# Kernel optimization log

Measured on AMD Instinct MI355X. Metric: run time of the kernel, lower is better.

The kernel has to match this reference:

```python
import jax, jax.numpy as jnp
import numpy as np

VIDEO_DIM, TEXT_DIM, ATTN_DIM = 1024, 768, 512
B, S1, S2 = 8, 256, 64


def setup_inputs() -> dict:
    key = jax.random.key(0)
    ks = jax.random.split(key, 10)
    return {
        "video": jax.random.normal(ks[0], (B, S1, VIDEO_DIM), dtype=jnp.float32),
        "text": jax.random.normal(ks[1], (B, S2, TEXT_DIM), dtype=jnp.float32),
        "video_mask": jax.random.randint(ks[2], (B, S1), 0, 2, dtype=jnp.int32),
        "text_mask": jax.random.randint(ks[3], (B, S2), 0, 2, dtype=jnp.int32),
        "w1": jax.random.normal(ks[4], (VIDEO_DIM, ATTN_DIM), dtype=jnp.float32),
        "w2": jax.random.normal(ks[5], (TEXT_DIM, ATTN_DIM), dtype=jnp.float32),
        "w3": jax.random.normal(ks[6], (ATTN_DIM, 1), dtype=jnp.float32),
        "bias": jax.random.normal(ks[7], (ATTN_DIM,), dtype=jnp.float32),
        "w4": jax.random.normal(ks[8], (ATTN_DIM * 4, 500), dtype=jnp.float32),
        "b4": jax.random.normal(ks[9], (500,), dtype=jnp.float32),
    }


def reference(video, text, video_mask, text_mask, w1, w2, w3, bias, w4, b4):
    # NOTE: original torch code calls h.masked_fill(...) (non in-place) and
    # discards the result, so video_mask/text_mask have NO effect. Faithful.
    # Project before broadcasting (mathematically identical to expand-then-matmul).
    h1 = jnp.einsum("bpd,da->bpa", video, w1)   # [b,s1,a]
    h2 = jnp.einsum("bqd,da->bqa", text, w2)    # [b,s2,a]
    # broadcast additive attention: [b,s1,s2,a]
    h = jnp.tanh(h1[:, :, None, :] + h2[:, None, :, :] + bias)
    e = jnp.einsum("bpqa,ao->bpq", h, w3)       # [b,s1,s2] (w3 has out-dim 1)
    # softmax over text dim (dim=2); the expand to attn_dim is uniform, so
    # softmax per-channel equals softmax of the scalar score.
    scores = jax.nn.softmax(e, axis=2)          # [b,s1,s2]
    text_attn = jnp.einsum("bpq,bqa->bpa", scores, h2)  # [b,s1,a]
    hh = h1                                      # video @ w1, same projection
    cont = jnp.concatenate([hh, text_attn, hh * text_attn, hh - text_attn], axis=-1)
    ret = jnp.einsum("bpc,co->bpo", jnp.tanh(cont), w4) + b4
    return ret
```

## Files before the change

### kernel.cpp

```cpp
#include <hip/hip_runtime.h>
#include <hip/hip_bf16.h>
#include <cstddef>

#define MBP   2048
#define MT    512
#define ADIM  512
#define VDIM  1024
#define TDIM  768
#define NOUT  500
#define CDIM  2048

typedef __attribute__((ext_vector_type(8))) short short8;
typedef __attribute__((ext_vector_type(4))) float floatx4;

__device__ __forceinline__ float tanh_fast(float x) {
    float e = __builtin_amdgcn_exp2f(x * 2.88539008177793f);
    float r = __builtin_amdgcn_rcpf(e + 1.0f);
    return __builtin_fmaf(-2.0f, r, 1.0f);
}

__device__ __forceinline__ unsigned short bf16r(float x) {
    union { float f; unsigned int u; } c; c.f = x;
    unsigned int r = (c.u + 0x7fffu + ((c.u >> 16) & 1u)) >> 16;
    return (unsigned short)r;
}
__device__ __forceinline__ float bf2f(unsigned short h) {
    union { unsigned int u; float f; } c; c.u = ((unsigned int)h) << 16;
    return c.f;
}

__device__ __forceinline__ void conv_split_body(
    const float* __restrict__ src, unsigned short* __restrict__ hi,
    unsigned short* __restrict__ lo, int blk)
{
    int i = blk * 256 + threadIdx.x;
    float4 v = ((const float4*)src)[i];
    ushort4 h, l;
    h.x = bf16r(v.x); l.x = bf16r(v.x - bf2f(h.x));
    h.y = bf16r(v.y); l.y = bf16r(v.y - bf2f(h.y));
    h.z = bf16r(v.z); l.z = bf16r(v.z - bf2f(h.z));
    h.w = bf16r(v.w); l.w = bf16r(v.w - bf2f(h.w));
    ((ushort4*)hi)[i] = h;
    ((ushort4*)lo)[i] = l;
}

__device__ __forceinline__ void transp_split_body(
    float (*tile)[33], const float* __restrict__ src,
    unsigned short* __restrict__ hi, unsigned short* __restrict__ lo,
    int R, int C, int bx, int by)
{
    const int tx = threadIdx.x & 31, ty = threadIdx.x >> 5;
    const int r0 = bx * 32, c0 = by * 32;
    #pragma unroll
    for (int i = 0; i < 4; ++i) {
        int r = r0 + ty + i * 8, c = c0 + tx;
        if (r < R && c < C) tile[ty + i * 8][tx] = src[(size_t)r * C + c];
    }
    __syncthreads();
    #pragma unroll
    for (int i = 0; i < 4; ++i) {
        int c = c0 + ty + i * 8, r = r0 + tx;
        if (c < C && r < R) {
            float v = tile[tx][ty + i * 8];
            unsigned short h = bf16r(v);
            hi[(size_t)c * R + r] = h;
            lo[(size_t)c * R + r] = bf16r(v - bf2f(h));
        }
    }
}

__device__ __forceinline__ void transp_single_body(
    float (*tile)[33], const float* __restrict__ src,
    unsigned short* __restrict__ dst, int R, int C, int bx, int by)
{
    const int tx = threadIdx.x & 31, ty = threadIdx.x >> 5;
    const int r0 = bx * 32, c0 = by * 32;
    #pragma unroll
    for (int i = 0; i < 4; ++i) {
        int r = r0 + ty + i * 8, c = c0 + tx;
        if (r < R && c < C) tile[ty + i * 8][tx] = src[(size_t)r * C + c];
    }
    __syncthreads();
    #pragma unroll
    for (int i = 0; i < 4; ++i) {
        int c = c0 + ty + i * 8, r = r0 + tx;
        if (c < C && r < R) dst[(size_t)c * R + r] = bf16r(tile[tx][ty + i * 8]);
    }
}

__global__ __launch_bounds__(256) void prep(
    const float* __restrict__ video, const float* __restrict__ text,
    const float* __restrict__ w1, const float* __restrict__ w2,
    const float* __restrict__ w4,
    unsigned short* __restrict__ vid_h, unsigned short* __restrict__ vid_l,
    unsigned short* __restrict__ txt_h, unsigned short* __restrict__ txt_l,
    unsigned short* __restrict__ w1t_h, unsigned short* __restrict__ w1t_l,
    unsigned short* __restrict__ w2t_h, unsigned short* __restrict__ w2t_l,
    unsigned short* __restrict__ w4t)
{
    __shared__ float tile[32][33];
    const int bid = blockIdx.x;
    if (bid < 2048) {
        conv_split_body(video, vid_h, vid_l, bid);
    } else if (bid < 2432) {
        conv_split_body(text, txt_h, txt_l, bid - 2048);
    } else if (bid < 2944) {
        int idx = bid - 2432;
        transp_split_body(tile, w1, w1t_h, w1t_l, VDIM, ADIM, idx & 31, idx >> 5);
    } else if (bid < 3328) {
        int idx = bid - 2944;
        transp_split_body(tile, w2, w2t_h, w2t_l, TDIM, ADIM, idx % 24, idx / 24);
    } else {
        int idx = bid - 3328;
        transp_single_body(tile, w4, w4t, CDIM, NOUT, idx & 63, idx >> 6);
    }
}

#define LP 40

__global__ __launch_bounds__(256) void gemm3_both(
    const unsigned short* __restrict__ vid_h, const unsigned short* __restrict__ vid_l,
    const unsigned short* __restrict__ w1t_h, const unsigned short* __restrict__ w1t_l,
    const unsigned short* __restrict__ txt_h, const unsigned short* __restrict__ txt_l,
    const unsigned short* __restrict__ w2t_h, const unsigned short* __restrict__ w2t_l,
    float* __restrict__ h1, float* __restrict__ h2,
    unsigned short* __restrict__ h2t_h, unsigned short* __restrict__ h2t_l)
{
    __shared__ __align__(16) unsigned short Ahs[2][64 * LP];
    __shared__ __align__(16) unsigned short Als[2][64 * LP];
    __shared__ __align__(16) unsigned short Bhs[2][64 * LP];
    __shared__ __align__(16) unsigned short Bls[2][64 * LP];

    const bool isH2 = (blockIdx.x >= 32);
    const unsigned short *Ah, *Al, *Bh, *Bl;
    float* C;
    int K, row0;
    if (!isH2) { Ah = vid_h; Al = vid_l; Bh = w1t_h; Bl = w1t_l; C = h1; K = VDIM; row0 = blockIdx.x * 64; }
    else       { Ah = txt_h; Al = txt_l; Bh = w2t_h; Bl = w2t_l; C = h2; K = TDIM; row0 = (blockIdx.x - 32) * 64; }

    const int t = threadIdx.x;
    const int r  = t >> 2;
    const int kc = (t & 3) << 3;
    const int col0 = blockIdx.y * 64;
    const int wave = t >> 6, lane = t & 63;
    const int m15 = lane & 15, q8 = (lane >> 4) << 3;

    const size_t aoff = (size_t)(row0 + r) * K + kc;
    const size_t boff = (size_t)(col0 + r) * K + kc;

    floatx4 acc[4] = { {0.f,0.f,0.f,0.f}, {0.f,0.f,0.f,0.f},
                       {0.f,0.f,0.f,0.f}, {0.f,0.f,0.f,0.f} };

    uint4 avh = *(const uint4*)(Ah + aoff);
    uint4 avl = *(const uint4*)(Al + aoff);
    uint4 bvh = *(const uint4*)(Bh + boff);
    uint4 bvl = *(const uint4*)(Bl + boff);
    *(uint4*)&Ahs[0][r * LP + kc] = avh;
    *(uint4*)&Als[0][r * LP + kc] = avl;
    *(uint4*)&Bhs[0][r * LP + kc] = bvh;
    *(uint4*)&Bls[0][r * LP + kc] = bvl;

    const int nIter = K >> 5;
    for (int i = 0; i < nIter; ++i) {
        __syncthreads();
        if (i + 1 < nIter) {
            int k0 = (i + 1) << 5;
            avh = *(const uint4*)(Ah + aoff + k0);
            avl = *(const uint4*)(Al + aoff + k0);
            bvh = *(const uint4*)(Bh + boff + k0);
            bvl = *(const uint4*)(Bl + boff + k0);
        }
        const int cur = i & 1;
        short8 afh = *(const short8*)&Ahs[cur][(wave * 16 + m15) * LP + q8];
        short8 afl = *(const short8*)&Als[cur][(wave * 16 + m15) * LP + q8];
        #pragma unroll
        for (int j = 0; j < 4; ++j) {
            short8 bfh = *(const short8*)&Bhs[cur][(j * 16 + m15) * LP + q8];
            short8 bfl = *(const short8*)&Bls[cur][(j * 16 + m15) * LP + q8];
            acc[j] = __builtin_amdgcn_mfma_f32_16x16x32_bf16(afh, bfh, acc[j], 0, 0, 0);
            acc[j] = __builtin_amdgcn_mfma_f32_16x16x32_bf16(afh, bfl, acc[j], 0, 0, 0);
            acc[j] = __builtin_amdgcn_mfma_f32_16x16x32_bf16(afl, bfh, acc[j], 0, 0, 0);
        }
        if (i + 1 < nIter) {
            const int nxt = cur ^ 1;
            *(uint4*)&Ahs[nxt][r * LP + kc] = avh;
            *(uint4*)&Als[nxt][r * LP + kc] = avl;
            *(uint4*)&Bhs[nxt][r * LP + kc] = bvh;
            *(uint4*)&Bls[nxt][r * LP + kc] = bvl;
        }
    }

    const int rbase = row0 + wave * 16 + (q8 >> 1);
    #pragma unroll
    for (int j = 0; j < 4; ++j) {
        int col = col0 + j * 16 + m15;
        #pragma unroll
        for (int rr = 0; rr < 4; ++rr) {
            int row = rbase + rr;
            float v = acc[j][rr];
            C[(size_t)row * ADIM + col] = v;
            if (isH2) {
                size_t idx = (size_t)(row >> 6) * (ADIM * 64) + (size_t)col * 64 + (row & 63);
                unsigned short h = bf16r(v);
                h2t_h[idx] = h;
                h2t_l[idx] = bf16r(v - bf2f(h));
            }
        }
    }
}

__global__ __launch_bounds__(256) void gemm_bf16(
    const unsigned short* __restrict__ A, const unsigned short* __restrict__ Bt,
    const float* __restrict__ bias, float* __restrict__ C,
    int M, int N, int K)
{
    __shared__ __align__(16) unsigned short As[2][64 * LP];
    __shared__ __align__(16) unsigned short Bs[2][64 * LP];

    const int t = threadIdx.x;
    const int r  = t >> 2;
    const int kc = (t & 3) << 3;
    const int row0 = blockIdx.x * 64, col0 = blockIdx.y * 64;
    const int wave = t >> 6, lane = t & 63;
    const int m15 = lane & 15, q8 = (lane >> 4) << 3;

    const unsigned short* Ap = A + (size_t)(row0 + r) * K + kc;
    const int bn = col0 + r;
    const unsigned short* Bp = Bt + (size_t)bn * K + kc;
    const bool bvalid = (bn < N);

    floatx4 acc[4] = { {0.f,0.f,0.f,0.f}, {0.f,0.f,0.f,0.f},
                       {0.f,0.f,0.f,0.f}, {0.f,0.f,0.f,0.f} };

    uint4 av = *(const uint4*)Ap;
    uint4 bv = {0u,0u,0u,0u};
    if (bvalid) bv = *(const uint4*)Bp;
    *(uint4*)&As[0][r * LP + kc] = av;
    *(uint4*)&Bs[0][r * LP + kc] = bv;

    const int nIter = K >> 5;
    for (int i = 0; i < nIter; ++i) {
        __syncthreads();
        if (i + 1 < nIter) {
            int k0 = (i + 1) << 5;
            av = *(const uint4*)(Ap + k0);
            if (bvalid) bv = *(const uint4*)(Bp + k0);
        }
        const int cur = i & 1;
        short8 af = *(const short8*)&As[cur][(wave * 16 + m15) * LP + q8];
        #pragma unroll
        for (int j = 0; j < 4; ++j) {
            short8 bf = *(const short8*)&Bs[cur][(j * 16 + m15) * LP + q8];
            acc[j] = __builtin_amdgcn_mfma_f32_16x16x32_bf16(af, bf, acc[j], 0, 0, 0);
        }
        if (i + 1 < nIter) {
            const int nxt = cur ^ 1;
            *(uint4*)&As[nxt][r * LP + kc] = av;
            *(uint4*)&Bs[nxt][r * LP + kc] = bv;
        }
    }

    const int rbase = row0 + wave * 16 + (q8 >> 1);
    #pragma unroll
    for (int j = 0; j < 4; ++j) {
        int col = col0 + j * 16 + m15;
        if (col < N) {
            float bvadd = bias ? bias[col] : 0.0f;
            #pragma unroll
            for (int rr = 0; rr < 4; ++rr)
                C[(size_t)(rbase + rr) * N + col] = acc[j][rr] + bvadd;
        }
    }
}

#define NP 4
#define TA 128
__global__ __launch_bounds__(256) void attn_scores(
    const float* __restrict__ h1,
    const float* __restrict__ h2,
    const float* __restrict__ bias,
    const float* __restrict__ w3,
    unsigned short* __restrict__ sc_h,
    unsigned short* __restrict__ sc_l)
{
    __shared__ __align__(16) float  h2t[TA / 4][64][4];
    __shared__ __align__(16) float2 h1bw[NP][ADIM];

    const int bp0 = blockIdx.x * NP;
    const int b   = bp0 >> 8;
    const int t   = threadIdx.x;
    const int wave = t >> 6, lane = t & 63;
    const float* h2b = h2 + (size_t)b * 64 * ADIM;

    for (int i = t; i < NP * ADIM; i += 256) {
        int p = i >> 9, a = i & 511;
        h1bw[p][a] = make_float2(h1[(size_t)(bp0 + p) * ADIM + a] + bias[a], w3[a]);
    }

    float acc = 0.f;
    for (int tile = 0; tile < ADIM / TA; ++tile) {
        const int a0 = tile * TA;
        __syncthreads();
        #pragma unroll
        for (int i = 0; i < TA / (NP * 4); ++i) {
            int a4 = (wave * (TA / (NP * 4)) + i) * 4;
            float4 v = *(const float4*)(h2b + (size_t)lane * ADIM + a0 + a4);
            *(float4*)&h2t[a4 >> 2][lane][0] = v;
        }
        __syncthreads();
        const float2* bw = &h1bw[wave][a0];
        #pragma unroll 8
        for (int g = 0; g < TA / 4; ++g) {
            float4 hv = *(const float4*)&h2t[g][lane][0];
            float2 c0 = bw[g * 4 + 0], c1 = bw[g * 4 + 1];
            float2 c2 = bw[g * 4 + 2], c3 = bw[g * 4 + 3];
            acc = __builtin_fmaf(tanh_fast(c0.x + hv.x), c0.y, acc);
            acc = __builtin_fmaf(tanh_fast(c1.x + hv.y), c1.y, acc);
            acc = __builtin_fmaf(tanh_fast(c2.x + hv.z), c2.y, acc);
            acc = __builtin_fmaf(tanh_fast(c3.x + hv.w), c3.y, acc);
        }
    }

    float m = acc;
    #pragma unroll
    for (int off = 32; off; off >>= 1) m = fmaxf(m, __shfl_xor(m, off, 64));
    float ex = __builtin_amdgcn_exp2f((acc - m) * 1.44269504088896f);
    float s = ex;
    #pragma unroll
    for (int off = 32; off; off >>= 1) s += __shfl_xor(s, off, 64);
    float sc = ex * __builtin_amdgcn_rcpf(s);
    unsigned short h = bf16r(sc);
    size_t oidx = (size_t)(bp0 + wave) * 64 + lane;
    sc_h[oidx] = h;
    sc_l[oidx] = bf16r(sc - bf2f(h));
}

__global__ __launch_bounds__(256) void ta_cont(
    const unsigned short* __restrict__ sc_h,
    const unsigned short* __restrict__ sc_l,
    const unsigned short* __restrict__ h2t_h,
    const unsigned short* __restrict__ h2t_l,
    const float* __restrict__ h1,
    unsigned short* __restrict__ tcont)
{
    const int row0 = blockIdx.x * 64;
    const int col0 = blockIdx.y * 64;
    const int b = row0 >> 8;
    const int t = threadIdx.x;
    const int wave = t >> 6, lane = t & 63;
    const int m15 = lane & 15, q8 = (lane >> 4) << 3;

    const size_t aidx = (size_t)(row0 + wave * 16 + m15) * 64 + q8;
    short8 af0h = *(const short8*)&sc_h[aidx];
    short8 af1h = *(const short8*)&sc_h[aidx + 32];
    short8 af0l = *(const short8*)&sc_l[aidx];
    short8 af1l = *(const short8*)&sc_l[aidx + 32];
    const size_t bbase = (size_t)b * ADIM * 64;

    floatx4 acc[4];
    #pragma unroll
    for (int j = 0; j < 4; ++j) {
        size_t boff = bbase + (size_t)(col0 + j * 16 + m15) * 64 + q8;
        short8 bf0h = *(const short8*)&h2t_h[boff];
        short8 bf1h = *(const short8*)&h2t_h[boff + 32];
        short8 bf0l = *(const short8*)&h2t_l[boff];
        short8 bf1l = *(const short8*)&h2t_l[boff + 32];
        floatx4 z = {0.f, 0.f, 0.f, 0.f};
        z = __builtin_amdgcn_mfma_f32_16x16x32_bf16(af0h, bf0h, z, 0, 0, 0);
        z = __builtin_amdgcn_mfma_f32_16x16x32_bf16(af0h, bf0l, z, 0, 0, 0);
        z = __builtin_amdgcn_mfma_f32_16x16x32_bf16(af0l, bf0h, z, 0, 0, 0);
        z = __builtin_amdgcn_mfma_f32_16x16x32_bf16(af1h, bf1h, z, 0, 0, 0);
        z = __builtin_amdgcn_mfma_f32_16x16x32_bf16(af1h, bf1l, z, 0, 0, 0);
        acc[j] = __builtin_amdgcn_mfma_f32_16x16x32_bf16(af1l, bf1h, z, 0, 0, 0);
    }

    const int rbase = row0 + wave * 16 + (q8 >> 1);
    #pragma unroll
    for (int j = 0; j < 4; ++j) {
        int a = col0 + j * 16 + m15;
        #pragma unroll
        for (int rr = 0; rr < 4; ++rr) {
            int row = rbase + rr;
            float ta = acc[j][rr];
            float hh = h1[(size_t)row * ADIM + a];
            unsigned short* o = tcont + (size_t)row * CDIM;
            o[a]            = bf16r(tanh_fast(hh));
            o[ADIM + a]     = bf16r(tanh_fast(ta));
            o[2 * ADIM + a] = bf16r(tanh_fast(hh * ta));
            o[3 * ADIM + a] = bf16r(tanh_fast(hh - ta));
        }
    }
}

extern "C" void kernel_launch(void* const* d_in, const int* in_sizes, int n_in,
                              void* d_out, int out_size, void* d_ws, size_t ws_size,
                              hipStream_t stream) {
    const float* video = (const float*)d_in[0];
    const float* text  = (const float*)d_in[1];
    const float* w1   = (const float*)d_in[4];
    const float* w2   = (const float*)d_in[5];
    const float* w3   = (const float*)d_in[6];
    const float* bias = (const float*)d_in[7];
    const float* w4   = (const float*)d_in[8];
    const float* b4   = (const float*)d_in[9];
    float* out = (float*)d_out;

    char* ws = (char*)d_ws;
    size_t off = 0;
    unsigned short* vid_h = (unsigned short*)(ws + off); off += (size_t)MBP * VDIM * 2;
    unsigned short* vid_l = (unsigned short*)(ws + off); off += (size_t)MBP * VDIM * 2;
    unsigned short* txt_h = (unsigned short*)(ws + off); off += (size_t)MT * TDIM * 2;
    unsigned short* txt_l = (unsigned short*)(ws + off); off += (size_t)MT * TDIM * 2;
    unsigned short* w1t_h = (unsigned short*)(ws + off); off += (size_t)ADIM * VDIM * 2;
    unsigned short* w1t_l = (unsigned short*)(ws + off); off += (size_t)ADIM * VDIM * 2;
    unsigned short* w2t_h = (unsigned short*)(ws + off); off += (size_t)ADIM * TDIM * 2;
    unsigned short* w2t_l = (unsigned short*)(ws + off); off += (size_t)ADIM * TDIM * 2;
    unsigned short* w4t   = (unsigned short*)(ws + off); off += (size_t)NOUT * CDIM * 2;
    float*          h1    = (float*)(ws + off);          off += (size_t)MBP * ADIM * 4;
    float*          h2    = (float*)(ws + off);          off += (size_t)MT * ADIM * 4;
    unsigned short* sc_h  = (unsigned short*)(ws + off); off += (size_t)MBP * 64 * 2;
    unsigned short* sc_l  = (unsigned short*)(ws + off); off += (size_t)MBP * 64 * 2;
    unsigned short* h2t_h = (unsigned short*)(ws + off); off += (size_t)8 * ADIM * 64 * 2;
    unsigned short* h2t_l = (unsigned short*)(ws + off); off += (size_t)8 * ADIM * 64 * 2;
    unsigned short* tc    = (unsigned short*)(ws + off); off += (size_t)MBP * CDIM * 2;

    prep<<<4352, 256, 0, stream>>>(video, text, w1, w2, w4,
                                   vid_h, vid_l, txt_h, txt_l,
                                   w1t_h, w1t_l, w2t_h, w2t_l, w4t);

    gemm3_both<<<dim3(40, 8), 256, 0, stream>>>(vid_h, vid_l, w1t_h, w1t_l,
                                                txt_h, txt_l, w2t_h, w2t_l,
                                                h1, h2, h2t_h, h2t_l);

    attn_scores<<<MBP / NP, 256, 0, stream>>>(h1, h2, bias, w3, sc_h, sc_l);

    ta_cont<<<dim3(MBP / 64, ADIM / 64), 256, 0, stream>>>(sc_h, sc_l, h2t_h, h2t_l, h1, tc);

    gemm_bf16<<<dim3(MBP / 64, (NOUT + 63) / 64), 256, 0, stream>>>(tc, w4t, b4, out, MBP, NOUT, CDIM);
}
```

Baseline: 165.1 us.

## Fuse input splitting into GEMM, split-K projections and output GEMM, restructure scores

Video and text bf16 hi/lo splitting now happens inside the projection GEMM's load path, so the separate conversion pass and its workspace traffic are gone. The video projection uses split-K in two halves whose partial results are summed by later consumers. The final output GEMM uses split-K by four with a separate reduce-plus-bias kernel. The attention-score kernel is restructured so each wave owns one video position and accumulates all 64 text scores in registers, and scores are stored as fp32 and split to bf16 in ta_cont. These changes aim to raise parallelism and cut memory passes, at the cost of extra partial-sum buffers, an extra launch and higher register pressure.

```diff
diff --git a/kernel.cpp b/kernel.cpp
--- a/kernel.cpp
+++ b/kernel.cpp
@@ -29,19 +29,29 @@
     return c.f;
 }
 
-__device__ __forceinline__ void conv_split_body(
-    const float* __restrict__ src, unsigned short* __restrict__ hi,
-    unsigned short* __restrict__ lo, int blk)
-{
-    int i = blk * 256 + threadIdx.x;
-    float4 v = ((const float4*)src)[i];
-    ushort4 h, l;
-    h.x = bf16r(v.x); l.x = bf16r(v.x - bf2f(h.x));
-    h.y = bf16r(v.y); l.y = bf16r(v.y - bf2f(h.y));
-    h.z = bf16r(v.z); l.z = bf16r(v.z - bf2f(h.z));
-    h.w = bf16r(v.w); l.w = bf16r(v.w - bf2f(h.w));
-    ((ushort4*)hi)[i] = h;
-    ((ushort4*)lo)[i] = l;
+__device__ __forceinline__ void split8(float4 a, float4 b, uint4& h, uint4& l) {
+    float f[8] = {a.x, a.y, a.z, a.w, b.x, b.y, b.z, b.w};
+    unsigned int hu[8], lu[8];
+    #pragma unroll
+    for (int i = 0; i < 8; ++i) {
+        unsigned short hh = bf16r(f[i]);
+        hu[i] = hh;
+        lu[i] = bf16r(f[i] - bf2f(hh));
+    }
+    h.x = hu[0] | (hu[1] << 16);
+    h.y = hu[2] | (hu[3] << 16);
+    h.z = hu[4] | (hu[5] << 16);
+    h.w = hu[6] | (hu[7] << 16);
+    l.x = lu[0] | (lu[1] << 16);
+    l.y = lu[2] | (lu[3] << 16);
+    l.z = lu[4] | (lu[5] << 16);
+    l.w = lu[6] | (lu[7] << 16);
+}
+
+__device__ __forceinline__ void split8s(const float* p, short8& hh, short8& ll) {
+    float4 a = *(const float4*)p, b = *(const float4*)(p + 4);
+    uint4 h, l; split8(a, b, h, l);
+    hh = *(short8*)&h; ll = *(short8*)&l;
 }
 
 __device__ __forceinline__ void transp_split_body(
@@ -89,41 +99,32 @@
 }
 
 __global__ __launch_bounds__(256) void prep(
-    const float* __restrict__ video, const float* __restrict__ text,
     const float* __restrict__ w1, const float* __restrict__ w2,
     const float* __restrict__ w4,
-    unsigned short* __restrict__ vid_h, unsigned short* __restrict__ vid_l,
-    unsigned short* __restrict__ txt_h, unsigned short* __restrict__ txt_l,
     unsigned short* __restrict__ w1t_h, unsigned short* __restrict__ w1t_l,
     unsigned short* __restrict__ w2t_h, unsigned short* __restrict__ w2t_l,
     unsigned short* __restrict__ w4t)
 {
     __shared__ float tile[32][33];
     const int bid = blockIdx.x;
-    if (bid < 2048) {
-        conv_split_body(video, vid_h, vid_l, bid);
-    } else if (bid < 2432) {
-        conv_split_body(text, txt_h, txt_l, bid - 2048);
-    } else if (bid < 2944) {
-        int idx = bid - 2432;
-        transp_split_body(tile, w1, w1t_h, w1t_l, VDIM, ADIM, idx & 31, idx >> 5);
-    } else if (bid < 3328) {
-        int idx = bid - 2944;
+    if (bid < 512) {
+        transp_split_body(tile, w1, w1t_h, w1t_l, VDIM, ADIM, bid & 31, bid >> 5);
+    } else if (bid < 896) {
+        int idx = bid - 512;
         transp_split_body(tile, w2, w2t_h, w2t_l, TDIM, ADIM, idx % 24, idx / 24);
     } else {
-        int idx = bid - 3328;
-        transp_single_body(tile, w4, w4t, CDIM, NOUT, idx & 63, idx >> 6);
+        int idx = bid - 896;
+        transp_single_body(tile, w4, w4t, CDIM, NOUT, idx >> 4, idx & 15);
     }
 }
 
 #define LP 40
 
 __global__ __launch_bounds__(256) void gemm3_both(
-    const unsigned short* __restrict__ vid_h, const unsigned short* __restrict__ vid_l,
+    const float* __restrict__ video, const float* __restrict__ text,
     const unsigned short* __restrict__ w1t_h, const unsigned short* __restrict__ w1t_l,
-    const unsigned short* __restrict__ txt_h, const unsigned short* __restrict__ txt_l,
     const unsigned short* __restrict__ w2t_h, const unsigned short* __restrict__ w2t_l,
-    float* __restrict__ h1, float* __restrict__ h2,
+    float* __restrict__ h1p, float* __restrict__ h2,
     unsigned short* __restrict__ h2t_h, unsigned short* __restrict__ h2t_l)
 {
     __shared__ __align__(16) unsigned short Ahs[2][64 * LP];
@@ -131,12 +132,22 @@
     __shared__ __align__(16) unsigned short Bhs[2][64 * LP];
     __shared__ __align__(16) unsigned short Bls[2][64 * LP];
 
-    const bool isH2 = (blockIdx.x >= 32);
-    const unsigned short *Ah, *Al, *Bh, *Bl;
+    const int bx = blockIdx.x;
+    const bool isH2 = (bx >= 64);
+    const float* Afp; const unsigned short *Bh, *Bl;
     float* C;
-    int K, row0;
-    if (!isH2) { Ah = vid_h; Al = vid_l; Bh = w1t_h; Bl = w1t_l; C = h1; K = VDIM; row0 = blockIdx.x * 64; }
-    else       { Ah = txt_h; Al = txt_l; Bh = w2t_h; Bl = w2t_l; C = h2; K = TDIM; row0 = (blockIdx.x - 32) * 64; }
+    int Kfull, kbase, nIter, row0;
+    if (!isH2) {
+        Afp = video; Bh = w1t_h; Bl = w1t_l;
+        Kfull = VDIM; kbase = (bx >> 5) * 512; nIter = 16;
+        row0 = (bx & 31) * 64;
+        C = h1p + (size_t)(bx >> 5) * MBP * ADIM;
+    } else {
+        Afp = text; Bh = w2t_h; Bl = w2t_l;
+        Kfull = TDIM; kbase = 0; nIter = 24;
+        row0 = (bx - 64) * 64;
+        C = h2;
+    }
 
     const int t = threadIdx.x;
     const int r  = t >> 2;
@@ -145,28 +156,30 @@
     const int wave = t >> 6, lane = t & 63;
     const int m15 = lane & 15, q8 = (lane >> 4) << 3;
 
-    const size_t aoff = (size_t)(row0 + r) * K + kc;
-    const size_t boff = (size_t)(col0 + r) * K + kc;
+    const size_t aoff = (size_t)(row0 + r) * Kfull + kbase + kc;
+    const size_t boff = (size_t)(col0 + r) * Kfull + kbase + kc;
 
     floatx4 acc[4] = { {0.f,0.f,0.f,0.f}, {0.f,0.f,0.f,0.f},
                        {0.f,0.f,0.f,0.f}, {0.f,0.f,0.f,0.f} };
 
-    uint4 avh = *(const uint4*)(Ah + aoff);
-    uint4 avl = *(const uint4*)(Al + aoff);
+    float4 a0 = *(const float4*)(Afp + aoff);
+    float4 a1 = *(const float4*)(Afp + aoff + 4);
     uint4 bvh = *(const uint4*)(Bh + boff);
     uint4 bvl = *(const uint4*)(Bl + boff);
-    *(uint4*)&Ahs[0][r * LP + kc] = avh;
-    *(uint4*)&Als[0][r * LP + kc] = avl;
-    *(uint4*)&Bhs[0][r * LP + kc] = bvh;
-    *(uint4*)&Bls[0][r * LP + kc] = bvl;
-
-    const int nIter = K >> 5;
+    {
+        uint4 avh, avl; split8(a0, a1, avh, avl);
+        *(uint4*)&Ahs[0][r * LP + kc] = avh;
+        *(uint4*)&Als[0][r * LP + kc] = avl;
+        *(uint4*)&Bhs[0][r * LP + kc] = bvh;
+        *(uint4*)&Bls[0][r * LP + kc] = bvl;
+    }
+
     for (int i = 0; i < nIter; ++i) {
         __syncthreads();
         if (i + 1 < nIter) {
             int k0 = (i + 1) << 5;
-            avh = *(const uint4*)(Ah + aoff + k0);
-            avl = *(const uint4*)(Al + aoff + k0);
+            a0 = *(const float4*)(Afp + aoff + k0);
+            a1 = *(const float4*)(Afp + aoff + k0 + 4);
             bvh = *(const uint4*)(Bh + boff + k0);
             bvl = *(const uint4*)(Bl + boff + k0);
         }
@@ -183,6 +196,7 @@
         }
         if (i + 1 < nIter) {
             const int nxt = cur ^ 1;
+            uint4 avh, avl; split8(a0, a1, avh, avl);
             *(uint4*)&Ahs[nxt][r * LP + kc] = avh;
             *(uint4*)&Als[nxt][r * LP + kc] = avl;
             *(uint4*)&Bhs[nxt][r * LP + kc] = bvh;
@@ -209,138 +223,80 @@
     }
 }
 
-__global__ __launch_bounds__(256) void gemm_bf16(
-    const unsigned short* __restrict__ A, const unsigned short* __restrict__ Bt,
-    const float* __restrict__ bias, float* __restrict__ C,
-    int M, int N, int K)
-{
-    __shared__ __align__(16) unsigned short As[2][64 * LP];
-    __shared__ __align__(16) unsigned short Bs[2][64 * LP];
-
-    const int t = threadIdx.x;
-    const int r  = t >> 2;
-    const int kc = (t & 3) << 3;
-    const int row0 = blockIdx.x * 64, col0 = blockIdx.y * 64;
-    const int wave = t >> 6, lane = t & 63;
-    const int m15 = lane & 15, q8 = (lane >> 4) << 3;
-
-    const unsigned short* Ap = A + (size_t)(row0 + r) * K + kc;
-    const int bn = col0 + r;
-    const unsigned short* Bp = Bt + (size_t)bn * K + kc;
-    const bool bvalid = (bn < N);
-
-    floatx4 acc[4] = { {0.f,0.f,0.f,0.f}, {0.f,0.f,0.f,0.f},
-                       {0.f,0.f,0.f,0.f}, {0.f,0.f,0.f,0.f} };
-
-    uint4 av = *(const uint4*)Ap;
-    uint4 bv = {0u,0u,0u,0u};
-    if (bvalid) bv = *(const uint4*)Bp;
-    *(uint4*)&As[0][r * LP + kc] = av;
-    *(uint4*)&Bs[0][r * LP + kc] = bv;
-
-    const int nIter = K >> 5;
-    for (int i = 0; i < nIter; ++i) {
-        __syncthreads();
-        if (i + 1 < nIter) {
-            int k0 = (i + 1) << 5;
-            av = *(const uint4*)(Ap + k0);
-            if (bvalid) bv = *(const uint4*)(Bp + k0);
-        }
-        const int cur = i & 1;
-        short8 af = *(const short8*)&As[cur][(wave * 16 + m15) * LP + q8];
-        #pragma unroll
-        for (int j = 0; j < 4; ++j) {
-            short8 bf = *(const short8*)&Bs[cur][(j * 16 + m15) * LP + q8];
-            acc[j] = __builtin_amdgcn_mfma_f32_16x16x32_bf16(af, bf, acc[j], 0, 0, 0);
-        }
-        if (i + 1 < nIter) {
-            const int nxt = cur ^ 1;
-            *(uint4*)&As[nxt][r * LP + kc] = av;
-            *(uint4*)&Bs[nxt][r * LP + kc] = bv;
-        }
-    }
-
-    const int rbase = row0 + wave * 16 + (q8 >> 1);
-    #pragma unroll
-    for (int j = 0; j < 4; ++j) {
-        int col = col0 + j * 16 + m15;
-        if (col < N) {
-            float bvadd = bias ? bias[col] : 0.0f;
-            #pragma unroll
-            for (int rr = 0; rr < 4; ++rr)
-                C[(size_t)(rbase + rr) * N + col] = acc[j][rr] + bvadd;
-        }
-    }
-}
-
-#define NP 4
-#define TA 128
-__global__ __launch_bounds__(256) void attn_scores(
-    const float* __restrict__ h1,
+__global__ __launch_bounds__(256, 4) void attn_scores(
+    const float* __restrict__ h1p,
     const float* __restrict__ h2,
     const float* __restrict__ bias,
     const float* __restrict__ w3,
-    unsigned short* __restrict__ sc_h,
-    unsigned short* __restrict__ sc_l)
-{
-    __shared__ __align__(16) float  h2t[TA / 4][64][4];
-    __shared__ __align__(16) float2 h1bw[NP][ADIM];
-
-    const int bp0 = blockIdx.x * NP;
+    float* __restrict__ sc)
+{
+    __shared__ float h2s[64][132];
+
+    const int bp0 = blockIdx.x * 4;
     const int b   = bp0 >> 8;
-    const int t   = threadIdx.x;
-    const int wave = t >> 6, lane = t & 63;
-    const float* h2b = h2 + (size_t)b * 64 * ADIM;
-
-    for (int i = t; i < NP * ADIM; i += 256) {
-        int p = i >> 9, a = i & 511;
-        h1bw[p][a] = make_float2(h1[(size_t)(bp0 + p) * ADIM + a] + bias[a], w3[a]);
-    }
-
-    float acc = 0.f;
-    for (int tile = 0; tile < ADIM / TA; ++tile) {
-        const int a0 = tile * TA;
+    const int t   = threadIdx.x, wave = t >> 6, lane = t & 63;
+    const int p   = bp0 + wave;
+    const float* h2b  = h2 + (size_t)b * 64 * ADIM;
+    const float* h1a  = h1p + (size_t)p * ADIM;
+    const float* h1b2 = h1p + (size_t)MBP * ADIM + (size_t)p * ADIM;
+
+    float acc[64];
+    #pragma unroll
+    for (int q = 0; q < 64; ++q) acc[q] = 0.f;
+
+    const int qrow = t >> 2, cch = t & 3;
+    #pragma unroll 1
+    for (int tile = 0; tile < 4; ++tile) {
+        const int a0 = tile * 128;
         __syncthreads();
         #pragma unroll
-        for (int i = 0; i < TA / (NP * 4); ++i) {
-            int a4 = (wave * (TA / (NP * 4)) + i) * 4;
-            float4 v = *(const float4*)(h2b + (size_t)lane * ADIM + a0 + a4);
-            *(float4*)&h2t[a4 >> 2][lane][0] = v;
+        for (int j = 0; j < 8; ++j) {
+            float4 v = *(const float4*)(h2b + (size_t)qrow * ADIM + a0 + (cch + 4 * j) * 4);
+            *(float4*)&h2s[qrow][(cch + 4 * j) * 4] = v;
         }
         __syncthreads();
-        const float2* bw = &h1bw[wave][a0];
-        #pragma unroll 8
-        for (int g = 0; g < TA / 4; ++g) {
-            float4 hv = *(const float4*)&h2t[g][lane][0];
-            float2 c0 = bw[g * 4 + 0], c1 = bw[g * 4 + 1];
-            float2 c2 = bw[g * 4 + 2], c3 = bw[g * 4 + 3];
-            acc = __builtin_fmaf(tanh_fast(c0.x + hv.x), c0.y, acc);
-            acc = __builtin_fmaf(tanh_fast(c1.x + hv.y), c1.y, acc);
-            acc = __builtin_fmaf(tanh_fast(c2.x + hv.z), c2.y, acc);
-            acc = __builtin_fmaf(tanh_fast(c3.x + hv.w), c3.y, acc);
-        }
-    }
-
-    float m = acc;
+        const int ag0 = a0 + lane, ag1 = ag0 + 64;
+        const float c0  = h1a[ag0] + h1b2[ag0] + bias[ag0];
+        const float c1  = h1a[ag1] + h1b2[ag1] + bias[ag1];
+        const float w30 = w3[ag0], w31 = w3[ag1];
+        const float* hp = &h2s[0][lane];
+        #pragma unroll
+        for (int q = 0; q < 64; ++q) {
+            acc[q] = __builtin_fmaf(tanh_fast(c0 + hp[q * 132]),      w30, acc[q]);
+            acc[q] = __builtin_fmaf(tanh_fast(c1 + hp[q * 132 + 64]), w31, acc[q]);
+        }
+    }
+    __syncthreads();
+
+    float* scr = &h2s[0][0] + wave * 2112;
+    float e = 0.f;
+    #pragma unroll 1
+    for (int hf = 0; hf < 2; ++hf) {
+        #pragma unroll
+        for (int q = 0; q < 32; ++q) scr[lane * 33 + q] = acc[hf * 32 + q];
+        float part = 0.f;
+        const int qq = lane & 31, r0 = (lane >> 5) * 32;
+        #pragma unroll
+        for (int j = 0; j < 32; ++j) part += scr[(r0 + j) * 33 + qq];
+        part += __shfl_xor(part, 32, 64);
+        if ((lane >> 5) == hf) e = part;
+    }
+
+    float m = e;
     #pragma unroll
     for (int off = 32; off; off >>= 1) m = fmaxf(m, __shfl_xor(m, off, 64));
-    float ex = __builtin_amdgcn_exp2f((acc - m) * 1.44269504088896f);
+    float ex = __builtin_amdgcn_exp2f((e - m) * 1.44269504088896f);
     float s = ex;
     #pragma unroll
     for (int off = 32; off; off >>= 1) s += __shfl_xor(s, off, 64);
-    float sc = ex * __builtin_amdgcn_rcpf(s);
-    unsigned short h = bf16r(sc);
-    size_t oidx = (size_t)(bp0 + wave) * 64 + lane;
-    sc_h[oidx] = h;
-    sc_l[oidx] = bf16r(sc - bf2f(h));
+    sc[(size_t)p * 64 + lane] = ex * __builtin_amdgcn_rcpf(s);
 }
 
 __global__ __launch_bounds__(256) void ta_cont(
-    const unsigned short* __restrict__ sc_h,
-    const unsigned short* __restrict__ sc_l,
+    const float* __restrict__ sc32,
     const unsigned short* __restrict__ h2t_h,
     const unsigned short* __restrict__ h2t_l,
-    const float* __restrict__ h1,
+    const float* __restrict__ h1p,
     unsigned short* __restrict__ tcont)
 {
     const int row0 = blockIdx.x * 64;
@@ -350,11 +306,10 @@
     const int wave = t >> 6, lane = t & 63;
     const int m15 = lane & 15, q8 = (lane >> 4) << 3;
 
-    const size_t aidx = (size_t)(row0 + wave * 16 + m15) * 64 + q8;
-    short8 af0h = *(const short8*)&sc_h[aidx];
-    short8 af1h = *(const short8*)&sc_h[aidx + 32];
-    short8 af0l = *(const short8*)&sc_l[aidx];
-    short8 af1l = *(const short8*)&sc_l[aidx + 32];
+    const float* ap = sc32 + (size_t)(row0 + wave * 16 + m15) * 64;
+    short8 af0h, af0l, af1h, af1l;
+    split8s(ap + q8, af0h, af0l);
+    split8s(ap + q8 + 32, af1h, af1l);
     const size_t bbase = (size_t)b * ADIM * 64;
 
     floatx4 acc[4];
@@ -374,6 +329,8 @@
         acc[j] = __builtin_amdgcn_mfma_f32_16x16x32_bf16(af1l, bf1h, z, 0, 0, 0);
     }
 
+    const float* h1a  = h1p;
+    const float* h1b2 = h1p + (size_t)MBP * ADIM;
     const int rbase = row0 + wave * 16 + (q8 >> 1);
     #pragma unroll
     for (int j = 0; j < 4; ++j) {
@@ -382,7 +339,8 @@
         for (int rr = 0; rr < 4; ++rr) {
             int row = rbase + rr;
             float ta = acc[j][rr];
-            float hh = h1[(size_t)row * ADIM + a];
+            size_t hi = (size_t)row * ADIM + a;
+            float hh = h1a[hi] + h1b2[hi];
             unsigned short* o = tcont + (size_t)row * CDIM;
             o[a]            = bf16r(tanh_fast(hh));
             o[ADIM + a]     = bf16r(tanh_fast(ta));
@@ -390,6 +348,88 @@
             o[3 * ADIM + a] = bf16r(tanh_fast(hh - ta));
         }
     }
+}
+
+__global__ __launch_bounds__(256) void gemm_bf16(
+    const unsigned short* __restrict__ A, const unsigned short* __restrict__ Bt,
+    float* __restrict__ P)
+{
+    __shared__ __align__(16) unsigned short As[2][64 * LP];
+    __shared__ __align__(16) unsigned short Bs[2][64 * LP];
+
+    const int t = threadIdx.x;
+    const int r  = t >> 2;
+    const int kc = (t & 3) << 3;
+    const int row0 = blockIdx.x * 64, col0 = blockIdx.y * 64;
+    const int kbase = blockIdx.z * 512;
+    const int wave = t >> 6, lane = t & 63;
+    const int m15 = lane & 15, q8 = (lane >> 4) << 3;
+
+    const unsigned short* Ap = A + (size_t)(row0 + r) * CDIM + kbase + kc;
+    const int bn = col0 + r;
+    const unsigned short* Bp = Bt + (size_t)bn * CDIM + kbase + kc;
+    const bool bvalid = (bn < NOUT);
+
+    floatx4 acc[4] = { {0.f,0.f,0.f,0.f}, {0.f,0.f,0.f,0.f},
+                       {0.f,0.f,0.f,0.f}, {0.f,0.f,0.f,0.f} };
+
+    uint4 av = *(const uint4*)Ap;
+    uint4 bv = {0u,0u,0u,0u};
+    if (bvalid) bv = *(const uint4*)Bp;
+    *(uint4*)&As[0][r * LP + kc] = av;
+    *(uint4*)&Bs[0][r * LP + kc] = bv;
+
+    const int nIter = 16;
+    for (int i = 0; i < nIter; ++i) {
+        __syncthreads();
+        if (i + 1 < nIter) {
+            int k0 = (i + 1) << 5;
+            av = *(const uint4*)(Ap + k0);
+            if (bvalid) bv = *(const uint4*)(Bp + k0);
+        }
+        const int cur = i & 1;
+        short8 af = *(const short8*)&As[cur][(wave * 16 + m15) * LP + q8];
+        #pragma unroll
+        for (int j = 0; j < 4; ++j) {
+            short8 bf = *(const short8*)&Bs[cur][(j * 16 + m15) * LP + q8];
+            acc[j] = __builtin_amdgcn_mfma_f32_16x16x32_bf16(af, bf, acc[j], 0, 0, 0);
+        }
+        if (i + 1 < nIter) {
+            const int nxt = cur ^ 1;
+            *(uint4*)&As[nxt][r * LP + kc] = av;
+            *(uint4*)&Bs[nxt][r * LP + kc] = bv;
+        }
+    }
+
+    float* Pz = P + (size_t)blockIdx.z * MBP * 512;
+    const int rbase = row0 + wave * 16 + (q8 >> 1);
+    #pragma unroll
+    for (int j = 0; j < 4; ++j) {
+        int col = col0 + j * 16 + m15;
+        if (col < NOUT) {
+            #pragma unroll
+            for (int rr = 0; rr < 4; ++rr)
+                Pz[(size_t)(rbase + rr) * 512 + col] = acc[j][rr];
+        }
+    }
+}
+
+__global__ __launch_bounds__(256) void reduce_bias(
+    const float* __restrict__ P, const float* __restrict__ b4,
+    float* __restrict__ out)
+{
+    int i = blockIdx.x * 256 + threadIdx.x;
+    if (i >= MBP * (NOUT / 2)) return;
+    int row = i / (NOUT / 2);
+    int col = (i - row * (NOUT / 2)) * 2;
+    const float* p = P + (size_t)row * 512 + col;
+    float2 v = *(const float2*)(b4 + col);
+    #pragma unroll
+    for (int z = 0; z < 4; ++z) {
+        float2 q = *(const float2*)(p + (size_t)z * MBP * 512);
+        v.x += q.x; v.y += q.y;
+    }
+    *(float2*)(out + (size_t)row * NOUT + col) = v;
 }
 
 extern "C" void kernel_launch(void* const* d_in, const int* in_sizes, int n_in,
@@ -407,34 +447,29 @@
 
     char* ws = (char*)d_ws;
     size_t off = 0;
-    unsigned short* vid_h = (unsigned short*)(ws + off); off += (size_t)MBP * VDIM * 2;
-    unsigned short* vid_l = (unsigned short*)(ws + off); off += (size_t)MBP * VDIM * 2;
-    unsigned short* txt_h = (unsigned short*)(ws + off); off += (size_t)MT * TDIM * 2;
-    unsigned short* txt_l = (unsigned short*)(ws + off); off += (size_t)MT * TDIM * 2;
     unsigned short* w1t_h = (unsigned short*)(ws + off); off += (size_t)ADIM * VDIM * 2;
     unsigned short* w1t_l = (unsigned short*)(ws + off); off += (size_t)ADIM * VDIM * 2;
     unsigned short* w2t_h = (unsigned short*)(ws + off); off += (size_t)ADIM * TDIM * 2;
     unsigned short* w2t_l = (unsigned short*)(ws + off); off += (size_t)ADIM * TDIM * 2;
     unsigned short* w4t   = (unsigned short*)(ws + off); off += (size_t)NOUT * CDIM * 2;
-    float*          h1    = (float*)(ws + off);          off += (size_t)MBP * ADIM * 4;
+    float*          h1p   = (float*)(ws + off);          off += (size_t)2 * MBP * ADIM * 4;
     float*          h2    = (float*)(ws + off);          off += (size_t)MT * ADIM * 4;
-    unsigned short* sc_h  = (unsigned short*)(ws + off); off += (size_t)MBP * 64 * 2;
-    unsigned short* sc_l  = (unsigned short*)(ws + off); off += (size_t)MBP * 64 * 2;
     unsigned short* h2t_h = (unsigned short*)(ws + off); off += (size_t)8 * ADIM * 64 * 2;
     unsigned short* h2t_l = (unsigned short*)(ws + off); off += (size_t)8 * ADIM * 64 * 2;
+    float*          sc32  = (float*)(ws + off);          off += (size_t)MBP * 64 * 4;
     unsigned short* tc    = (unsigned short*)(ws + off); off += (size_t)MBP * CDIM * 2;
-
-    prep<<<4352, 256, 0, stream>>>(video, text, w1, w2, w4,
-                                   vid_h, vid_l, txt_h, txt_l,
-                                   w1t_h, w1t_l, w2t_h, w2t_l, w4t);
-
-    gemm3_both<<<dim3(40, 8), 256, 0, stream>>>(vid_h, vid_l, w1t_h, w1t_l,
-                                                txt_h, txt_l, w2t_h, w2t_l,
-                                                h1, h2, h2t_h, h2t_l);
-
-    attn_scores<<<MBP / NP, 256, 0, stream>>>(h1, h2, bias, w3, sc_h, sc_l);
-
-    ta_cont<<<dim3(MBP / 64, ADIM / 64), 256, 0, stream>>>(sc_h, sc_l, h2t_h, h2t_l, h1, tc);
-
-    gemm_bf16<<<dim3(MBP / 64, (NOUT + 63) / 64), 256, 0, stream>>>(tc, w4t, b4, out, MBP, NOUT, CDIM);
-}
+    float*          gpart = (float*)(ws + off);          off += (size_t)4 * MBP * 512 * 4;
+
+    prep<<<1920, 256, 0, stream>>>(w1, w2, w4, w1t_h, w1t_l, w2t_h, w2t_l, w4t);
+
+    gemm3_both<<<dim3(72, 8), 256, 0, stream>>>(video, text, w1t_h, w1t_l,
+                                                w2t_h, w2t_l, h1p, h2, h2t_h, h2t_l);
+
+    attn_scores<<<MBP / 4, 256, 0, stream>>>(h1p, h2, bias, w3, sc32);
+
+    ta_cont<<<dim3(MBP / 64, ADIM / 64), 256, 0, stream>>>(sc32, h2t_h, h2t_l, h1p, tc);
+
+    gemm_bf16<<<dim3(MBP / 64, 8, 4), 256, 0, stream>>>(tc, w4t, gpart);
+
+    reduce_bias<<<(MBP * (NOUT / 2) + 255) / 256, 256, 0, stream>>>(gpart, b4, out);
+}
```

Measured after the change: 175.8 us. 6.5% more time.
